# Performance work log

Measured on AMD Instinct MI355X. Metric: run time of the kernel, lower is better.

## Reference

```python
import jax, jax.numpy as jnp
import numpy as np

BS, F, C, H, W = 2, 8, 64, 128, 128
HEADS = 4

def build_edges(bs, f):
    rows, cols, ec = [], [], 0
    for b in range(bs):
        s = b * (2 * f + 2)
        v = list(range(s, s + f)); d = list(range(s + f, s + 2 * f))
        t = s + 2 * f; g = t + 1
        for grp in (v, d, v + d, v + d, v + d + [t], [t], [g]):
            rows += grp; cols += [ec] * len(grp); ec += 1
    return np.asarray(rows, np.int32), np.asarray(cols, np.int32), ec

ROW, COL, NUM_EDGES = build_edges(BS, F)

def conv2d_s2(x, w, b):  # Conv2d k3 s2 p1 + ReLU
    y = jax.lax.conv_general_dilated(x, w, (2, 2), [(1, 1), (1, 1)],
        dimension_numbers=('NCHW', 'OIHW', 'NCHW'))
    return jax.nn.relu(y + b[None, :, None, None])

def conv_t2(x, w, b):  # ConvTranspose2d k3 s2 p1 op1 + ReLU; w: (in,out,3,3)
    wt = jnp.flip(w, (2, 3)).transpose(1, 0, 2, 3)
    y = jax.lax.conv_general_dilated(x, wt, (1, 1), [(1, 2), (1, 2)],
        lhs_dilation=(2, 2), dimension_numbers=('NCHW', 'OIHW', 'NCHW'))
    return jax.nn.relu(y + b[None, :, None, None])

def layer_norm(x, eps=1e-5):  # affine params are default ones/zeros
    mu = x.mean(-1, keepdims=True)
    var = ((x - mu) ** 2).mean(-1, keepdims=True)
    return (x - mu) / jnp.sqrt(var + eps)

def group_norm(x, groups=32, eps=1e-5):
    n, c = x.shape
    xg = x.reshape(n, groups, c // groups)
    mu = xg.mean(-1, keepdims=True)
    var = ((xg - mu) ** 2).mean(-1, keepdims=True)
    return ((xg - mu) / jnp.sqrt(var + eps)).reshape(n, c)

def se_layer(x, w1, w2):  # squeeze over node dim 0
    y = jax.nn.sigmoid(jax.nn.relu(x.mean(0) @ w1.T) @ w2.T)
    return x * y

def hypergraph_conv(x, lin_w, att, edge_w, edge_attr, out_ch):
    # PyG HypergraphConv, use_attention=True, attention_mode='node', heads=4,
    # concat=False, bias=False, eval mode (dropout inactive)
    n = x.shape[0]
    xl = (x @ lin_w.T).reshape(n, HEADS, out_ch)
    ea = (edge_attr @ lin_w.T).reshape(-1, HEADS, out_ch)
    a = (jnp.concatenate([xl[ROW], ea[COL]], axis=-1) * att).sum(-1)  # (E, heads)
    a = jax.nn.leaky_relu(a, 0.2)
    a = jnp.exp(a - jax.ops.segment_max(a, COL, num_segments=NUM_EDGES)[COL])
    a = a / (jax.ops.segment_sum(a, COL, num_segments=NUM_EDGES)[COL] + 1e-16)
    D = jax.ops.segment_sum(edge_w[COL], ROW, num_segments=n)
    D = jnp.where(D > 0, 1.0 / D, 0.0)
    B = jax.ops.segment_sum(jnp.ones(ROW.shape[0], x.dtype), COL, num_segments=NUM_EDGES)
    B = jnp.where(B > 0, 1.0 / B, 0.0)
    e = jax.ops.segment_sum(B[COL][:, None, None] * a[:, :, None] * xl[ROW], COL, num_segments=NUM_EDGES)
    o = jax.ops.segment_sum(D[ROW][:, None, None] * a[:, :, None] * e[COL], ROW, num_segments=n)
    return o.mean(1)  # concat=False -> head mean

def setup_inputs() -> dict:
    key = jax.random.key(0)
    ks = jax.random.split(key, 32)
    def n(k, shape, s=1.0):
        return jax.random.normal(k, shape, jnp.float32) * s
    def u(k, shape):
        return jax.random.uniform(k, shape, jnp.float32)
    return {
        'vision_feat': n(ks[0], (BS, F, C, H, W)), 'vision_pos': n(ks[1], (BS, F, C, H, W), 0.1),
        'motion_feat': n(ks[2], (BS, F, C, H, W)), 'motion_pos': n(ks[3], (BS, F, C, H, W), 0.1),
        'text_feat': n(ks[4], (BS, C, 16)), 'text_pos': n(ks[5], (BS, C, 16), 0.1),
        'cv1_w': n(ks[6], (2 * C, C, 3, 3), 0.04), 'cv1_b': n(ks[7], (2 * C,), 0.01),
        'cv2_w': n(ks[8], (4 * C, 2 * C, 3, 3), 0.03), 'cv2_b': n(ks[9], (4 * C,), 0.01),
        'dc1_w': n(ks[10], (2 * C, C, 3, 3), 0.04), 'dc1_b': n(ks[11], (2 * C,), 0.01),
        'dc2_w': n(ks[12], (4 * C, 2 * C, 3, 3), 0.03), 'dc2_b': n(ks[13], (4 * C,), 0.01),
        'tc1_w': n(ks[14], (4 * C, 2 * C, 3, 3), 0.03), 'tc1_b': n(ks[15], (2 * C,), 0.01),
        'tc2_w': n(ks[16], (2 * C, C, 3, 3), 0.04), 'tc2_b': n(ks[17], (C,), 0.01),
        'lin1_w': n(ks[18], (HEADS * 8 * C, 4 * C), 0.06), 'att1': n(ks[19], (1, HEADS, 16 * C), 0.05),
        'lin2_w': n(ks[20], (HEADS * 4 * C, 8 * C), 0.04), 'att2': n(ks[21], (1, HEADS, 8 * C), 0.05),
        'ew1': u(ks[22], (2 * F * BS + 2,)), 'ew2': u(ks[23], (2 * F * BS + 2,)),
        'ea1': u(ks[24], (2 * F * BS + 2, 4 * C)), 'ea2': u(ks[25], (2 * F * BS + 2, 8 * C)),
        'se1_w1': n(ks[26], (8 * C // 16, 8 * C), 0.06), 'se1_w2': n(ks[27], (8 * C, 8 * C // 16), 0.15),
        'se2_w1': n(ks[28], (4 * C // 16, 4 * C), 0.08), 'se2_w2': n(ks[29], (4 * C, 4 * C // 16), 0.2),
    }

def reference(vision_feat, vision_pos, motion_feat, motion_pos, text_feat, text_pos,
              cv1_w, cv1_b, cv2_w, cv2_b, dc1_w, dc1_b, dc2_w, dc2_b,
              tc1_w, tc1_b, tc2_w, tc2_b, lin1_w, att1, lin2_w, att2,
              ew1, ew2, ea1, ea2, se1_w1, se1_w2, se2_w1, se2_w2):
    bs, f, c, h, w = vision_feat.shape
    # text_pool: AdaptiveMaxPool1d(4) on L=16 -> exact windows of 4; view(bs,-1)
    tn = (text_feat + text_pos).reshape(bs, c, 4, 4).max(-1).reshape(bs, 4 * c)
    v0 = (vision_feat + vision_pos).reshape(bs * f, c, h, w)
    v1 = conv2d_s2(v0, cv1_w, cv1_b)          # (bs*f, 2c, h/2, w/2)
    v2 = conv2d_s2(v1, cv2_w, cv2_b)          # (bs*f, 4c, h/4, w/4)
    vn = layer_norm(v2.max((2, 3)))           # AdaptiveMaxPool2d(1) + LayerNorm
    d0 = (motion_feat + motion_pos).reshape(bs * f, c, h, w)
    dn = layer_norm(conv2d_s2(conv2d_s2(d0, dc1_w, dc1_b), dc2_w, dc2_b).max((2, 3)))
    vb = vn.reshape(bs, f, 4 * c); db = dn.reshape(bs, f, 4 * c)
    obs = tn + (vb + db).mean(1)              # observer = mean(text+v+d) over frames
    x = jnp.concatenate([vb, db, tn[:, None], obs[:, None]], axis=1).reshape(bs * (2 * f + 2), 4 * c)
    x = se_layer(group_norm(jax.nn.relu(hypergraph_conv(x, lin1_w, att1, ew1, ea1, 8 * c))), se1_w1, se1_w2)
    x = se_layer(group_norm(jax.nn.relu(hypergraph_conv(x, lin2_w, att2, ew2, ea2, 4 * c))), se2_w1, se2_w2)
    xb = x.reshape(bs, 2 * f + 2, 4 * c)
    # obs_pool: AdaptiveMaxPool1d(c) on L=4c -> windows of 4
    observers = (tn + xb[:, -1]).reshape(bs, c, 4).max(-1)
    vg = xb[:, :f].reshape(bs * f, 4 * c)
    # bilinear upsample of 1x1 == broadcast; transconv doubles size so the
    # subsequent F.interpolate calls to (h/2,w/2) and (h,w) are identities
    vr = v2 + vg[:, :, None, None]
    vr = v1 + conv_t2(vr, tc1_w, tc1_b)
    vr = v0 + conv_t2(vr, tc2_w, tc2_b)
    return vr, observers
```

## Files before the change

kernel.cpp:

```cpp
#include <hip/hip_runtime.h>
#include <hip/hip_bf16.h>
#include <cstddef>
#include <cstdint>

#define DEV_INLINE __device__ __forceinline__
#define AS1 __attribute__((address_space(1)))
#define AS3 __attribute__((address_space(3)))

typedef __attribute__((ext_vector_type(8))) short short8;
typedef __attribute__((ext_vector_type(4))) float f32x4;
typedef __attribute__((ext_vector_type(2))) float f32x2;
typedef __attribute__((ext_vector_type(4))) unsigned short us4;

DEV_INLINE unsigned short f2bf(float f) {
  uint32_t u = __builtin_bit_cast(uint32_t, f);
  uint32_t r = (u + 0x7fffu + ((u >> 16) & 1u)) >> 16;
  return (unsigned short)r;
}
DEV_INLINE float bf2f(unsigned short u) {
  return __builtin_bit_cast(float, (uint32_t)u << 16);
}

DEV_INLINE void gl_lds16(const float* g, float* l) {
  __builtin_amdgcn_global_load_lds((AS1 void*)const_cast<float*>(g),
                                   (AS3 void*)l, 16, 0, 0);
}

__device__ __constant__ int c_cs[15] = {0,8,16,32,48,65,66,67,75,83,99,115,132,133,134};
__device__ __constant__ int c_row[134] = {
  0,1,2,3,4,5,6,7,
  8,9,10,11,12,13,14,15,
  0,1,2,3,4,5,6,7,8,9,10,11,12,13,14,15,
  0,1,2,3,4,5,6,7,8,9,10,11,12,13,14,15,
  0,1,2,3,4,5,6,7,8,9,10,11,12,13,14,15,16,
  16,
  17,
  18,19,20,21,22,23,24,25,
  26,27,28,29,30,31,32,33,
  18,19,20,21,22,23,24,25,26,27,28,29,30,31,32,33,
  18,19,20,21,22,23,24,25,26,27,28,29,30,31,32,33,
  18,19,20,21,22,23,24,25,26,27,28,29,30,31,32,33,34,
  34,
  35
};
__device__ __constant__ int c_col[134] = {
  0,0,0,0,0,0,0,0,
  1,1,1,1,1,1,1,1,
  2,2,2,2,2,2,2,2,2,2,2,2,2,2,2,2,
  3,3,3,3,3,3,3,3,3,3,3,3,3,3,3,3,
  4,4,4,4,4,4,4,4,4,4,4,4,4,4,4,4,4,
  5,
  6,
  7,7,7,7,7,7,7,7,
  8,8,8,8,8,8,8,8,
  9,9,9,9,9,9,9,9,9,9,9,9,9,9,9,9,
  10,10,10,10,10,10,10,10,10,10,10,10,10,10,10,10,
  11,11,11,11,11,11,11,11,11,11,11,11,11,11,11,11,11,
  12,
  13
};

__global__ __launch_bounds__(512) void k_prep(const float* __restrict__ a,
                                              const float* __restrict__ b,
                                              unsigned short* __restrict__ o) {
  __shared__ float sbuf[32 * 260];
  int bid = blockIdx.x;
  int y = bid & 127, n = bid >> 7;
  int t = threadIdx.x;
  int w = t >> 6, lane = t & 63;
  int cio = lane >> 5;
  int xg4 = (lane & 31) * 4;
  const size_t base = ((size_t)n * 64) * 16384 + (size_t)y * 128;
#pragma unroll
  for (int k = 0; k < 4; ++k) {
    int c = w * 4 + k;
    gl_lds16(a + base + (size_t)(2 * c + cio) * 16384 + xg4, &sbuf[c * 260]);
  }
  __syncthreads();
  auto rd = [&](int ci, int x) {
    return sbuf[(ci >> 1) * 260 + (ci & 1) * 128 + x];
  };
  float av[2][8];
#pragma unroll
  for (int it = 0; it < 2; ++it) {
    int i = t + it * 512;
    int x = i >> 3, cq = i & 7;
#pragma unroll
    for (int j = 0; j < 8; ++j) av[it][j] = rd(cq * 8 + j, x);
  }
  __syncthreads();
#pragma unroll
  for (int k = 0; k < 4; ++k) {
    int c = w * 4 + k;
    gl_lds16(b + base + (size_t)(2 * c + cio) * 16384 + xg4, &sbuf[c * 260]);
  }
  __syncthreads();
  unsigned int* op = (unsigned int*)(o + (((size_t)n * 128 + y) * 128) * 64);
#pragma unroll
  for (int it = 0; it < 2; ++it) {
    int i = t + it * 512;
    int x = i >> 3, cq = i & 7;
    uint4 v;
    unsigned int vv[4];
#pragma unroll
    for (int jj = 0; jj < 4; ++jj) {
      unsigned int lo = f2bf(av[it][2 * jj]     + rd(cq * 8 + 2 * jj, x));
      unsigned int hi = f2bf(av[it][2 * jj + 1] + rd(cq * 8 + 2 * jj + 1, x));
      vv[jj] = lo | (hi << 16);
    }
    v.x = vv[0]; v.y = vv[1]; v.z = vv[2]; v.w = vv[3];
    *reinterpret_cast<uint4*>(op + x * 32 + cq * 4) = v;
  }
}

__global__ void k_wtrans_all(const float* __restrict__ cv1w, const float* __restrict__ dc1w,
                             const float* __restrict__ cv2w, const float* __restrict__ dc2w,
                             const float* __restrict__ tc1w, const float* __restrict__ tc2w,
                             unsigned short* __restrict__ wtb) {
  int idx = blockIdx.x * 256 + threadIdx.x;
  const float* src; int off, lci, lco; bool tra;
  if (idx < 73728)        { src = cv1w; off = 0;       lci = 6; lco = 7; tra = false; }
  else if (idx < 147456)  { src = dc1w; off = 73728;   lci = 6; lco = 7; tra = false; }
  else if (idx < 442368)  { src = cv2w; off = 147456;  lci = 7; lco = 8; tra = false; }
  else if (idx < 737280)  { src = dc2w; off = 442368;  lci = 7; lco = 8; tra = false; }
  else if (idx < 1032192) { src = tc1w; off = 737280;  lci = 8; lco = 7; tra = true;  }
  else if (idx < 1105920) { src = tc2w; off = 1032192; lci = 7; lco = 6; tra = true;  }
  else return;
  int l = idx - off;
  int ci = l & ((1 << lci) - 1);
  int r = l >> lci;
  int co = r & ((1 << lco) - 1);
  int tap = r >> lco;
  size_t si = tra ? (((size_t)ci << lco) + co) * 9 + tap
                  : (((size_t)co << lci) + ci) * 9 + tap;
  wtb[idx] = f2bf(src[si]);
}

template<int CI, int CO, int HO, int WO, int ROUT, bool SPLIT_IN>
__global__ __launch_bounds__(512, 3) void k_conv_mfma_b(
    const unsigned short* __restrict__ in0, const unsigned short* __restrict__ in1,
    const unsigned short* __restrict__ wT0, const unsigned short* __restrict__ wT1,
    const float* __restrict__ b0, const float* __restrict__ b1,
    unsigned short* __restrict__ outn) {
  constexpr int HIN = HO * 2, WIN = WO * 2;
  constexpr int XHP = WO + 2;
  constexpr int R = 2 * ROUT + 1;
  constexpr int NPOS = R * 2 * XHP;
  constexpr int NCH = NPOS * 4;
  constexpr int NCS = CI / 32;
  constexpr int KIT = (NCH + 511) / 512;
  constexpr int CB = CO / 128;
  constexpr int OB = HO / ROUT;
  __shared__ short8 sIn[NPOS * 5];
  int bid = blockIdx.x;
  int cb = bid % CB; bid /= CB;
  int oyb = bid % OB; int n = bid / OB;
  int br = n >> 4;
  const unsigned short* in = SPLIT_IN ? (br ? in1 : in0) : in0;
  const unsigned short* wT = br ? wT1 : wT0;
  const float* bias = br ? b1 : b0;
  int ni = SPLIT_IN ? (n & 15) : n;
  int tid = threadIdx.x;
  int wid = tid >> 6, lane = tid & 63;
  int wm = wid >> 1, wn = wid & 1;
  int llo = lane & 15, lhi = lane >> 4;
  f32x4 acc[2][2] = {};
  const int iy0 = oyb * (2 * ROUT) - 1;
  short8 rv[KIT];
  auto loadr = [&](int cs) {
#pragma unroll
    for (int k = 0; k < KIT; ++k) {
      int i = tid + k * 512;
      short8 v = {};
      if (i < NCH) {
        int c = i & 3, q = i >> 2;
        int xh = q % XHP; int q2 = q / XHP;
        int p = q2 & 1, l = q2 >> 1;
        int x = 2 * xh + p - 1;
        int iy = iy0 + l;
        if (x >= 0 && x < WIN && iy >= 0 && iy < HIN)
          v = *reinterpret_cast<const short8*>(in + ((((size_t)ni * HIN + iy) * WIN + x) * CI + cs * 32 + c * 8));
      }
      rv[k] = v;
    }
  };
  auto writes = [&]() {
#pragma unroll
    for (int k = 0; k < KIT; ++k) {
      int i = tid + k * 512;
      if (i < NCH) sIn[(i >> 2) * 5 + (i & 3)] = rv[k];
    }
  };
  loadr(0);
  for (int cs = 0; cs < NCS; ++cs) {
    writes();
    __syncthreads();
    if (cs + 1 < NCS) loadr(cs + 1);
    short8 afr9[9][2];
#pragma unroll
    for (int tap = 0; tap < 9; ++tap)
#pragma unroll
      for (int m = 0; m < 2; ++m) {
        int co = cb * 128 + wm * 32 + m * 16 + llo;
        afr9[tap][m] = *reinterpret_cast<const short8*>(wT + (((size_t)tap * CO + co) * CI + cs * 32 + lhi * 8));
      }
#pragma unroll
    for (int tap = 0; tap < 9; ++tap) {
      const int ky = tap / 3, kx = tap % 3;
      short8 bfr[2];
#pragma unroll
      for (int n2 = 0; n2 < 2; ++n2) {
        int pix = wn * 32 + n2 * 16 + llo;
        int oyl = (ROUT == 2) ? (pix >> 5) : 0;
        int ox = pix - oyl * WO;
        int lrow = 2 * oyl + ky;
        int pos = (lrow * 2 + (kx & 1)) * XHP + ox + (kx >> 1);
        bfr[n2] = sIn[pos * 5 + lhi];
      }
#pragma unroll
      for (int m = 0; m < 2; ++m)
#pragma unroll
        for (int n2 = 0; n2 < 2; ++n2)
          acc[m][n2] = __builtin_amdgcn_mfma_f32_16x16x32_bf16(afr9[tap][m], bfr[n2], acc[m][n2], 0, 0, 0);
    }
    __syncthreads();
  }
#pragma unroll
  for (int m = 0; m < 2; ++m) {
    int co0 = cb * 128 + wm * 32 + m * 16 + lhi * 4;
    f32x4 bv = *reinterpret_cast<const f32x4*>(bias + co0);
#pragma unroll
    for (int n2 = 0; n2 < 2; ++n2) {
      int pix = wn * 32 + n2 * 16 + llo;
      int oyl = (ROUT == 2) ? (pix >> 5) : 0;
      int ox = pix - oyl * WO;
      int oy = oyb * ROUT + oyl;
      us4 pk;
      pk[0] = f2bf(fmaxf(acc[m][n2][0] + bv[0], 0.f));
      pk[1] = f2bf(fmaxf(acc[m][n2][1] + bv[1], 0.f));
      pk[2] = f2bf(fmaxf(acc[m][n2][2] + bv[2], 0.f));
      pk[3] = f2bf(fmaxf(acc[m][n2][3] + bv[3], 0.f));
      *reinterpret_cast<us4*>(outn + ((((size_t)n * HO + oy) * WO + ox) * CO + co0)) = pk;
    }
  }
}

template<int CI, int CO, int Hi, int Wi, int QR, bool OBF, bool GADD>
__global__ __launch_bounds__(256, 3) void k_deconv_mfma(
    const unsigned short* __restrict__ in,
    const unsigned short* __restrict__ wT,
    const float* __restrict__ bias,
    const unsigned short* __restrict__ resn,
    const float* __restrict__ gsrc,
    unsigned short* __restrict__ outn,
    float* __restrict__ outc) {
  constexpr int QC = 64 / QR;
  constexpr int WP = Wi + 1;
  constexpr int NPOS = (QR + 1) * WP;
  constexpr int NCH = NPOS * 4;
  constexpr int NCS = CI / 32;
  constexpr int KIT = (NCH + 255) / 256;
  constexpr int CB = CO / 64;
  constexpr int OB = Hi / QR;
  constexpr int Ho = Hi * 2, Wo = Wi * 2;
  __shared__ short8 sIn[NPOS * 5];
  int bid = blockIdx.x;
  int cb = bid % CB; bid /= CB;
  int oyb = bid % OB; int n = bid / OB;
  int tid = threadIdx.x;
  int wid = tid >> 6, lane = tid & 63;
  int wm = wid >> 1, wn = wid & 1;
  int llo = lane & 15, lhi = lane >> 4;
  int qy0 = oyb * QR;
  const float* g = nullptr;
  if constexpr (GADD) g = gsrc + ((size_t)((n >> 3) * 18 + (n & 7))) * 256;
  f32x4 acc[4][2][2] = {};
  constexpr int tap_p[9] = {3,2,3,1,0,1,3,2,3};
  constexpr int tap_b[9] = {3,2,2,1,0,0,1,0,0};
  short8 rv[KIT];
  auto loadr = [&](int cs) {
#pragma unroll
    for (int k = 0; k < KIT; ++k) {
      int i = tid + k * 256;
      short8 v = {};
      if (i < NCH) {
        int c = i & 3, q = i >> 2;
        int x = q % WP, l = q / WP;
        int iy = qy0 + l;
        if (x < Wi && iy < Hi) {
          v = *reinterpret_cast<const short8*>(in + (((size_t)(n * Hi + iy) * Wi + x) * CI + cs * 32 + c * 8));
          if constexpr (GADD) {
#pragma unroll
            for (int j = 0; j < 8; ++j) {
              float fv = bf2f((unsigned short)v[j]) + g[cs * 32 + c * 8 + j];
              v[j] = (short)f2bf(fv);
            }
          }
        }
      }
      rv[k] = v;
    }
  };
  auto writes = [&]() {
#pragma unroll
    for (int k = 0; k < KIT; ++k) {
      int i = tid + k * 256;
      if (i < NCH) sIn[(i >> 2) * 5 + (i & 3)] = rv[k];
    }
  };
  loadr(0);
  for (int cs = 0; cs < NCS; ++cs) {
    writes();
    __syncthreads();
    if (cs + 1 < NCS) loadr(cs + 1);
    short8 bfr[2][4];
#pragma unroll
    for (int n2 = 0; n2 < 2; ++n2) {
      int pix = wn * 32 + n2 * 16 + llo;
      int qyl = pix / QC, qx = pix % QC;
#pragma unroll
      for (int bs = 0; bs < 4; ++bs) {
        int pos = (qyl + (bs >> 1)) * WP + qx + (bs & 1);
        bfr[n2][bs] = sIn[pos * 5 + lhi];
      }
    }
#pragma unroll
    for (int m = 0; m < 2; ++m) {
      short8 afr9[9];
#pragma unroll
      for (int tap = 0; tap < 9; ++tap) {
        int co = cb * 64 + wm * 32 + m * 16 + llo;
        afr9[tap] = *reinterpret_cast<const short8*>(wT + (((size_t)tap * CO + co) * CI + cs * 32 + lhi * 8));
      }
#pragma unroll
      for (int tap = 0; tap < 9; ++tap)
#pragma unroll
        for (int n2 = 0; n2 < 2; ++n2)
          acc[tap_p[tap]][m][n2] = __builtin_amdgcn_mfma_f32_16x16x32_bf16(
              afr9[tap], bfr[n2][tap_b[tap]], acc[tap_p[tap]][m][n2], 0, 0, 0);
    }
    __syncthreads();
  }
#pragma unroll
  for (int m = 0; m < 2; ++m) {
    int co0 = cb * 64 + wm * 32 + m * 16 + lhi * 4;
    f32x4 bv = *reinterpret_cast<const f32x4*>(bias + co0);
#pragma unroll
    for (int n2 = 0; n2 < 2; ++n2) {
      int pix = wn * 32 + n2 * 16 + llo;
      int qyl = pix / QC, qx = pix % QC;
      int qy = qy0 + qyl;
      if constexpr (OBF) {
#pragma unroll
        for (int p = 0; p < 4; ++p) {
          int oy = 2 * qy + (p >> 1);
          int ox = 2 * qx + (p & 1);
          size_t ad = ((size_t)(n * Ho + oy) * Wo + ox) * CO + co0;
          us4 r = *reinterpret_cast<const us4*>(resn + ad);
          us4 pk;
#pragma unroll
          for (int c = 0; c < 4; ++c)
            pk[c] = f2bf(bf2f(r[c]) + fmaxf(acc[p][m][n2][c] + bv[c], 0.f));
          *reinterpret_cast<us4*>(outn + ad) = pk;
        }
      } else {
        int qx2 = 2 * qx;
#pragma unroll
        for (int dy = 0; dy < 2; ++dy) {
          int oy = 2 * qy + dy;
          size_t rb = ((size_t)(n * Ho + oy) * Wo + qx2) * CO + co0;
          us4 r0 = *reinterpret_cast<const us4*>(resn + rb);
          us4 r1 = *reinterpret_cast<const us4*>(resn + rb + CO);
#pragma unroll
          for (int c = 0; c < 4; ++c) {
            f32x2 st;
            st[0] = bf2f(r0[c]) + fmaxf(acc[dy * 2][m][n2][c] + bv[c], 0.f);
            st[1] = bf2f(r1[c]) + fmaxf(acc[dy * 2 + 1][m][n2][c] + bv[c], 0.f);
            __builtin_nontemporal_store(st,
                reinterpret_cast<f32x2*>(outc + ((size_t)(n * CO + co0 + c) * Ho + oy) * Wo + qx2));
          }
        }
      }
    }
  }
}

__global__ __launch_bounds__(256) void k_max_part(const unsigned short* __restrict__ x,
                                                  float* __restrict__ pmax) {
  int n = blockIdx.x >> 3, pg = blockIdx.x & 7;
  int t = threadIdx.x;
  int c8 = t & 31;
  int ps = t >> 5;
  const unsigned short* base = x + (size_t)n * 262144 + (size_t)pg * 32768 + (size_t)c8 * 8;
  float m[8];
#pragma unroll
  for (int j = 0; j < 8; ++j) m[j] = -1e30f;
  for (int p = ps * 16; p < ps * 16 + 16; ++p) {
    short8 v = *reinterpret_cast<const short8*>(base + (size_t)p * 256);
#pragma unroll
    for (int j = 0; j < 8; ++j) m[j] = fmaxf(m[j], bf2f((unsigned short)v[j]));
  }
  __shared__ float sred[8][264];
#pragma unroll
  for (int j = 0; j < 8; ++j) sred[ps][c8 * 8 + j] = m[j];
  __syncthreads();
  float mm = sred[0][t];
#pragma unroll
  for (int g = 1; g < 8; ++g) mm = fmaxf(mm, sred[g][t]);
  pmax[((size_t)n * 8 + pg) * 256 + t] = mm;
}

__global__ __launch_bounds__(256) void k_ln(const float* __restrict__ pmax,
                                            float* __restrict__ out) {
  int n = blockIdx.x, ch = threadIdx.x;
  float m = -1e30f;
#pragma unroll
  for (int g = 0; g < 8; ++g)
    m = fmaxf(m, pmax[((size_t)n * 8 + g) * 256 + ch]);
  __shared__ float r1[256], r2[256];
  r1[ch] = m; __syncthreads();
  for (int s = 128; s > 0; s >>= 1) { if (ch < s) r1[ch] += r1[ch + s]; __syncthreads(); }
  float mu = r1[0] * (1.f / 256.f);
  float d = m - mu;
  r2[ch] = d * d; __syncthreads();
  for (int s = 128; s > 0; s >>= 1) { if (ch < s) r2[ch] += r2[ch + s]; __syncthreads(); }
  out[(size_t)n * 256 + ch] = d * rsqrtf(r2[0] * (1.f / 256.f) + 1e-5f);
}

__global__ void k_build_x(const float* __restrict__ tf, const float* __restrict__ tp,
                          const float* __restrict__ nb,
                          float* __restrict__ tn, float* __restrict__ x0) {
  int b = blockIdx.x, ch = threadIdx.x;
  int c4 = ch >> 2, j = ch & 3;
  const float* p = tf + ((size_t)b * 64 + c4) * 16 + j * 4;
  const float* q = tp + ((size_t)b * 64 + c4) * 16 + j * 4;
  float tv = p[0] + q[0];
  tv = fmaxf(tv, p[1] + q[1]);
  tv = fmaxf(tv, p[2] + q[2]);
  tv = fmaxf(tv, p[3] + q[3]);
  tn[(size_t)b * 256 + ch] = tv;
  const float* dn = nb;
  const float* vn = nb + 16 * 256;
  float s = 0.f;
  for (int f = 0; f < 8; ++f) {
    float vv = vn[((size_t)b * 8 + f) * 256 + ch];
    float dd = dn[((size_t)b * 8 + f) * 256 + ch];
    s += vv + dd;
    x0[((size_t)b * 18 + f) * 256 + ch] = vv;
    x0[((size_t)b * 18 + 8 + f) * 256 + ch] = dd;
  }
  x0[((size_t)b * 18 + 16) * 256 + ch] = tv;
  x0[((size_t)b * 18 + 17) * 256 + ch] = tv + s * (1.f / 8.f);
}

__global__ __launch_bounds__(256) void k_gnn_lin(
    const float* __restrict__ x, const float* __restrict__ ea,
    const float* __restrict__ w, float* __restrict__ y, int K, int M) {
  int chunks = M >> 8;
  int r = blockIdx.x / chunks;
  int ob = (blockIdx.x % chunks) * 256 + threadIdx.x;
  const float* src = (r < 36) ? (x + (size_t)r * K) : (ea + (size_t)(r - 36) * K);
  __shared__ __align__(16) float sxr[512];
  for (int k = threadIdx.x; k < K; k += 256) sxr[k] = src[k];
  __syncthreads();
  const float4* w4 = reinterpret_cast<const float4*>(w + (size_t)ob * K);
  const float4* x4 = reinterpret_cast<const float4*>(sxr);
  float acc = 0.f;
  int k4 = K >> 2;
  for (int k = 0; k < k4; ++k) {
    float4 a = x4[k], b = w4[k];
    acc += a.x * b.x + a.y * b.y + a.z * b.z + a.w * b.w;
  }
  y[(size_t)r * M + ob] = acc;
}

template<int OC>
__global__ __launch_bounds__(256) void k_gnn_attsm(
    const float* __restrict__ y, const float* __restrict__ att,
    float* __restrict__ attw) {
  int t = threadIdx.x;
  __shared__ float sx_s[144], seb_s[60];
  __shared__ float a_s[536];
  if (t < 200) {
    int r = t >> 2, h = t & 3;
    const float4* row = reinterpret_cast<const float4*>(y + ((size_t)r * 4 + h) * OC);
    const float4* ar = reinterpret_cast<const float4*>(att + (size_t)h * 2 * OC + (r < 36 ? 0 : OC));
    float s = 0.f;
#pragma unroll 4
    for (int k = 0; k < OC / 4; ++k) {
      float4 a = row[k], b = ar[k];
      s += a.x * b.x + a.y * b.y + a.z * b.z + a.w * b.w;
    }
    if (r < 36) sx_s[r * 4 + h] = s; else seb_s[(r - 36) * 4 + h] = s;
  }
  __syncthreads();
  for (int idx = t; idx < 536; idx += 256) {
    int i = idx >> 2, h = idx & 3;
    float v = sx_s[c_row[i] * 4 + h] + seb_s[c_col[i] * 4 + h];
    a_s[idx] = (v > 0.f) ? v : 0.2f * v;
  }
  __syncthreads();
  if (t < 56) {
    int c = t >> 2, h = t & 3;
    int st = c_cs[c], en = c_cs[c + 1];
    float m = -1e30f;
    for (int i = st; i < en; ++i) m = fmaxf(m, a_s[i * 4 + h]);
    float s = 0.f;
    for (int i = st; i < en; ++i) { float e = __expf(a_s[i * 4 + h] - m); a_s[i * 4 + h] = e; s += e; }
    float inv = 1.f / (s + 1e-16f);
    for (int i = st; i < en; ++i) a_s[i * 4 + h] *= inv;
  }
  __syncthreads();
  for (int idx = t; idx < 536; idx += 256) attw[idx] = a_s[idx];
}

template<int OC>
__global__ __launch_bounds__(256) void k_edge_agg(
    const float* __restrict__ y, const float* __restrict__ attw,
    float* __restrict__ eb) {
  int idx = blockIdx.x * 256 + threadIdx.x;
  if (idx >= 14 * 4 * OC) return;
  int ch = idx % OC;
  int h = (idx / OC) & 3;
  int c = idx / (4 * OC);
  int st = c_cs[c], en = c_cs[c + 1];
  float s = 0.f;
  for (int i = st; i < en; ++i)
    s += attw[i * 4 + h] * y[(size_t)c_row[i] * (4 * OC) + h * OC + ch];
  eb[idx] = s * (1.f / (float)(en - st));
}

template<int OC>
__global__ __launch_bounds__(256) void k_node_agg(
    const float* __restrict__ attw, const float* __restrict__ eb,
    const float* __restrict__ ew, float* __restrict__ ho) {
  int idx = blockIdx.x * 256 + threadIdx.x;
  if (idx >= 36 * OC) return;
  int ch = idx % OC;
  int node = idx / OC;
  int b = node / 18, ln = node % 18;
  int ncols, cols[4], gis[4];
  if (ln < 16) {
    ncols = 4;
    cols[0] = b * 7 + (ln < 8 ? 0 : 1); gis[0] = b * 67 + ln;
    cols[1] = b * 7 + 2; gis[1] = b * 67 + 16 + ln;
    cols[2] = b * 7 + 3; gis[2] = b * 67 + 32 + ln;
    cols[3] = b * 7 + 4; gis[3] = b * 67 + 48 + ln;
  } else if (ln == 16) {
    ncols = 2;
    cols[0] = b * 7 + 4; gis[0] = b * 67 + 64;
    cols[1] = b * 7 + 5; gis[1] = b * 67 + 65;
    cols[2] = cols[3] = 0; gis[2] = gis[3] = 0;
  } else {
    ncols = 1;
    cols[0] = b * 7 + 6; gis[0] = b * 67 + 66;
    cols[1] = cols[2] = cols[3] = 0; gis[1] = gis[2] = gis[3] = 0;
  }
  float dsum = 0.f;
#pragma unroll
  for (int k = 0; k < 4; ++k) if (k < ncols) dsum += ew[cols[k]];
  float D = dsum > 0.f ? 1.f / dsum : 0.f;
  float s = 0.f;
#pragma unroll
  for (int k = 0; k < 4; ++k) {
    if (k < ncols) {
#pragma unroll
      for (int h = 0; h < 4; ++h)
        s += attw[gis[k] * 4 + h] * eb[((size_t)cols[k] * 4 + h) * OC + ch];
    }
  }
  ho[idx] = fmaxf(0.25f * D * s, 0.f);
}

template<int C, int Cr>
__global__ __launch_bounds__(512) void k_gn_se(
    const float* __restrict__ hin, const float* __restrict__ w1,
    const float* __restrict__ w2, float* __restrict__ x) {
  int t = threadIdx.x;
  constexpr int gs = C >> 5;
  for (int idx = t; idx < 36 * 32; idx += 512) {
    int node = idx >> 5, g = idx & 31;
    const float* p = hin + (size_t)node * C + g * gs;
    float s = 0.f, s2 = 0.f;
#pragma unroll
    for (int k = 0; k < gs; ++k) { float v = p[k]; s += v; s2 += v * v; }
    float mu = s * (1.f / gs);
    float var = s2 * (1.f / gs) - mu * mu;
    float inv = rsqrtf(fmaxf(var, 0.f) + 1e-5f);
    float* q = x + (size_t)node * C + g * gs;
#pragma unroll
    for (int k = 0; k < gs; ++k) q[k] = (p[k] - mu) * inv;
  }
  __threadfence_block();
  __syncthreads();
  __shared__ float smean[C];
  __shared__ float spart[Cr][17];
  __shared__ float shid[Cr];
  __shared__ float sscale[C];
  if (t < C) {
    float s = 0.f;
    for (int nn = 0; nn < 36; ++nn) s += x[(size_t)nn * C + t];
    smean[t] = s * (1.f / 36.f);
  }
  __syncthreads();
  if (t < Cr * 16) {
    int hid = t >> 4, sub = t & 15;
    constexpr int CH = C / 16;
    float s = 0.f;
#pragma unroll
    for (int k = 0; k < CH; ++k)
      s += w1[(size_t)hid * C + sub * CH + k] * smean[sub * CH + k];
    spart[hid][sub] = s;
  }
  __syncthreads();
  if (t < Cr) {
    float s = 0.f;
#pragma unroll
    for (int k = 0; k < 16; ++k) s += spart[t][k];
    shid[t] = fmaxf(s, 0.f);
  }
  __syncthreads();
  if (t < C) {
    float s = 0.f;
#pragma unroll
    for (int k = 0; k < Cr; ++k) s += w2[(size_t)t * Cr + k] * shid[k];
    sscale[t] = 1.f / (1.f + __expf(-s));
  }
  __syncthreads();
  for (int idx = t; idx < 36 * C; idx += 512) x[idx] *= sscale[idx % C];
}

__global__ void k_obs(const float* __restrict__ tn, const float* __restrict__ x2,
                      float* __restrict__ out) {
  int t = threadIdx.x;
  if (t >= 128) return;
  int b = t >> 6, ch = t & 63;
  const float* a = tn + (size_t)b * 256 + ch * 4;
  const float* c = x2 + ((size_t)b * 18 + 17) * 256 + ch * 4;
  float m = a[0] + c[0];
  m = fmaxf(m, a[1] + c[1]);
  m = fmaxf(m, a[2] + c[2]);
  m = fmaxf(m, a[3] + c[3]);
  out[b * 64 + ch] = m;
}

extern "C" void kernel_launch(void* const* d_in, const int* in_sizes, int n_in,
                              void* d_out, int out_size, void* d_ws, size_t ws_size,
                              hipStream_t stream) {
  (void)in_sizes; (void)n_in; (void)out_size; (void)ws_size;
  const float* vf    = (const float*)d_in[0];
  const float* vp    = (const float*)d_in[1];
  const float* mf    = (const float*)d_in[2];
  const float* mp    = (const float*)d_in[3];
  const float* tf    = (const float*)d_in[4];
  const float* tp    = (const float*)d_in[5];
  const float* cv1w  = (const float*)d_in[6];
  const float* cv1b  = (const float*)d_in[7];
  const float* cv2w  = (const float*)d_in[8];
  const float* cv2b  = (const float*)d_in[9];
  const float* dc1w  = (const float*)d_in[10];
  const float* dc1b  = (const float*)d_in[11];
  const float* dc2w  = (const float*)d_in[12];
  const float* dc2b  = (const float*)d_in[13];
  const float* tc1w  = (const float*)d_in[14];
  const float* tc1b  = (const float*)d_in[15];
  const float* tc2w  = (const float*)d_in[16];
  const float* tc2b  = (const float*)d_in[17];
  const float* lin1w = (const float*)d_in[18];
  const float* att1  = (const float*)d_in[19];
  const float* lin2w = (const float*)d_in[20];
  const float* att2  = (const float*)d_in[21];
  const float* ew1   = (const float*)d_in[22];
  const float* ew2   = (const float*)d_in[23];
  const float* ea1   = (const float*)d_in[24];
  const float* ea2   = (const float*)d_in[25];
  const float* se1w1 = (const float*)d_in[26];
  const float* se1w2 = (const float*)d_in[27];
  const float* se2w1 = (const float*)d_in[28];
  const float* se2w2 = (const float*)d_in[29];

  float* ws  = (float*)d_ws;
  float* out = (float*)d_out;

  unsigned short* p0nm = (unsigned short*)(ws);
  unsigned short* p0nv = (unsigned short*)(ws + 8388608);
  unsigned short* q1nb = (unsigned short*)(ws + 16777216);
  unsigned short* wtb  = (unsigned short*)(ws + 25165824);
  float* sm   = ws + 25718784;
  float* tn   = sm;
  float* nb   = sm + 512;
  float* x0   = sm + 8704;
  float* xl   = sm + 17920;
  float* eb   = sm + 120520;
  float* ho   = sm + 149192;
  float* x1   = sm + 167624;
  float* x2   = sm + 186056;
  float* attw = sm + 195272;
  float* pmax = sm + 195904;

  unsigned short* v2nb = (unsigned short*)d_out;
  unsigned short* t1n = (unsigned short*)(ws);

  unsigned short* wTc1 = wtb;
  unsigned short* wTd1 = wtb + 73728;
  unsigned short* wTc2 = wtb + 147456;
  unsigned short* wTd2 = wtb + 442368;
  unsigned short* wTt1 = wtb + 737280;
  unsigned short* wTt2 = wtb + 1032192;

  k_wtrans_all<<<4320, 256, 0, stream>>>(cv1w, dc1w, cv2w, dc2w, tc1w, tc2w, wtb);

  k_prep<<<2048, 512, 0, stream>>>(mf, mp, p0nm);
  k_prep<<<2048, 512, 0, stream>>>(vf, vp, p0nv);

  k_conv_mfma_b<64, 128, 64, 64, 1, true><<<2048, 512, 0, stream>>>(
      p0nm, p0nv, wTd1, wTc1, dc1b, cv1b, q1nb);
  k_conv_mfma_b<128, 256, 32, 32, 2, false><<<1024, 512, 0, stream>>>(
      q1nb, nullptr, wTd2, wTc2, dc2b, cv2b, v2nb);
  k_max_part<<<256, 256, 0, stream>>>(v2nb, pmax);
  k_ln<<<32, 256, 0, stream>>>(pmax, nb);

  k_build_x<<<2, 256, 0, stream>>>(tf, tp, nb, tn, x0);

  k_gnn_lin<<<50 * 8, 256, 0, stream>>>(x0, ea1, lin1w, xl, 256, 2048);
  k_gnn_attsm<512><<<1, 256, 0, stream>>>(xl, att1, attw);
  k_edge_agg<512><<<112, 256, 0, stream>>>(xl, attw, eb);
  k_node_agg<512><<<72, 256, 0, stream>>>(attw, eb, ew1, ho);
  k_gn_se<512, 32><<<1, 512, 0, stream>>>(ho, se1w1, se1w2, x1);

  k_gnn_lin<<<50 * 4, 256, 0, stream>>>(x1, ea2, lin2w, xl, 512, 1024);
  k_gnn_attsm<256><<<1, 256, 0, stream>>>(xl, att2, attw);
  k_edge_agg<256><<<56, 256, 0, stream>>>(xl, attw, eb);
  k_node_agg<256><<<36, 256, 0, stream>>>(attw, eb, ew2, ho);
  k_gn_se<256, 16><<<1, 512, 0, stream>>>(ho, se2w1, se2w2, x2);

  k_obs<<<1, 128, 0, stream>>>(tn, x2, out + 16777216);

  unsigned short* v2nv = v2nb + 4194304;
  unsigned short* q1nv = q1nb + 8388608;
  k_deconv_mfma<256, 128, 32, 32, 2, true, true><<<512, 256, 0, stream>>>(
      v2nv, wTt1, tc1b, q1nv, x2, t1n, nullptr);
  k_deconv_mfma<128, 64, 64, 64, 1, false, false><<<1024, 256, 0, stream>>>(
      t1n, wTt2, tc2b, p0nv, nullptr, nullptr, out);
}
```

Before: 462.4 us.

## Drop LDS staging in stride-2 convs and load input fragments directly from global

```diff
diff --git a/kernel.cpp b/kernel.cpp
--- a/kernel.cpp
+++ b/kernel.cpp
@@ -137,21 +137,15 @@
 }
 
 template<int CI, int CO, int HO, int WO, int ROUT, bool SPLIT_IN>
-__global__ __launch_bounds__(512, 3) void k_conv_mfma_b(
+__global__ __launch_bounds__(512, 4) void k_conv_direct(
     const unsigned short* __restrict__ in0, const unsigned short* __restrict__ in1,
     const unsigned short* __restrict__ wT0, const unsigned short* __restrict__ wT1,
     const float* __restrict__ b0, const float* __restrict__ b1,
     unsigned short* __restrict__ outn) {
   constexpr int HIN = HO * 2, WIN = WO * 2;
-  constexpr int XHP = WO + 2;
-  constexpr int R = 2 * ROUT + 1;
-  constexpr int NPOS = R * 2 * XHP;
-  constexpr int NCH = NPOS * 4;
   constexpr int NCS = CI / 32;
-  constexpr int KIT = (NCH + 511) / 512;
   constexpr int CB = CO / 128;
   constexpr int OB = HO / ROUT;
-  __shared__ short8 sIn[NPOS * 5];
   int bid = blockIdx.x;
   int cb = bid % CB; bid /= CB;
   int oyb = bid % OB; int n = bid / OB;
@@ -164,66 +158,43 @@
   int wid = tid >> 6, lane = tid & 63;
   int wm = wid >> 1, wn = wid & 1;
   int llo = lane & 15, lhi = lane >> 4;
+  int ox_[2], iyb_[2];
+#pragma unroll
+  for (int n2 = 0; n2 < 2; ++n2) {
+    int pix = wn * 32 + n2 * 16 + llo;
+    int oyl = (ROUT == 2) ? (pix >> 5) : 0;
+    int ox = pix - oyl * WO;
+    int oy = oyb * ROUT + oyl;
+    ox_[n2] = ox;
+    iyb_[n2] = 2 * oy - 1;
+  }
   f32x4 acc[2][2] = {};
-  const int iy0 = oyb * (2 * ROUT) - 1;
-  short8 rv[KIT];
-  auto loadr = [&](int cs) {
-#pragma unroll
-    for (int k = 0; k < KIT; ++k) {
-      int i = tid + k * 512;
-      short8 v = {};
-      if (i < NCH) {
-        int c = i & 3, q = i >> 2;
-        int xh = q % XHP; int q2 = q / XHP;
-        int p = q2 & 1, l = q2 >> 1;
-        int x = 2 * xh + p - 1;
-        int iy = iy0 + l;
-        if (x >= 0 && x < WIN && iy >= 0 && iy < HIN)
-          v = *reinterpret_cast<const short8*>(in + ((((size_t)ni * HIN + iy) * WIN + x) * CI + cs * 32 + c * 8));
-      }
-      rv[k] = v;
-    }
-  };
-  auto writes = [&]() {
-#pragma unroll
-    for (int k = 0; k < KIT; ++k) {
-      int i = tid + k * 512;
-      if (i < NCH) sIn[(i >> 2) * 5 + (i & 3)] = rv[k];
-    }
-  };
-  loadr(0);
   for (int cs = 0; cs < NCS; ++cs) {
-    writes();
-    __syncthreads();
-    if (cs + 1 < NCS) loadr(cs + 1);
-    short8 afr9[9][2];
-#pragma unroll
-    for (int tap = 0; tap < 9; ++tap)
+    int kb = cs * 32 + lhi * 8;
+#pragma unroll
+    for (int tap = 0; tap < 9; ++tap) {
+      const int ky = tap / 3, kx = tap % 3;
+      short8 afr[2], bfr[2];
 #pragma unroll
       for (int m = 0; m < 2; ++m) {
         int co = cb * 128 + wm * 32 + m * 16 + llo;
-        afr9[tap][m] = *reinterpret_cast<const short8*>(wT + (((size_t)tap * CO + co) * CI + cs * 32 + lhi * 8));
+        afr[m] = *reinterpret_cast<const short8*>(wT + (((size_t)tap * CO + co) * CI + kb));
       }
 #pragma unroll
-    for (int tap = 0; tap < 9; ++tap) {
-      const int ky = tap / 3, kx = tap % 3;
-      short8 bfr[2];
-#pragma unroll
       for (int n2 = 0; n2 < 2; ++n2) {
-        int pix = wn * 32 + n2 * 16 + llo;
-        int oyl = (ROUT == 2) ? (pix >> 5) : 0;
-        int ox = pix - oyl * WO;
-        int lrow = 2 * oyl + ky;
-        int pos = (lrow * 2 + (kx & 1)) * XHP + ox + (kx >> 1);
-        bfr[n2] = sIn[pos * 5 + lhi];
+        int ix = 2 * ox_[n2] - 1 + kx;
+        int iy = iyb_[n2] + ky;
+        short8 v = {};
+        if (ix >= 0 && iy >= 0)
+          v = *reinterpret_cast<const short8*>(in + ((((size_t)ni * HIN + iy) * WIN + ix) * CI + kb));
+        bfr[n2] = v;
       }
 #pragma unroll
       for (int m = 0; m < 2; ++m)
 #pragma unroll
         for (int n2 = 0; n2 < 2; ++n2)
-          acc[m][n2] = __builtin_amdgcn_mfma_f32_16x16x32_bf16(afr9[tap][m], bfr[n2], acc[m][n2], 0, 0, 0);
-    }
-    __syncthreads();
+          acc[m][n2] = __builtin_amdgcn_mfma_f32_16x16x32_bf16(afr[m], bfr[n2], acc[m][n2], 0, 0, 0);
+    }
   }
 #pragma unroll
   for (int m = 0; m < 2; ++m) {
@@ -713,9 +684,9 @@
   k_prep<<<2048, 512, 0, stream>>>(mf, mp, p0nm);
   k_prep<<<2048, 512, 0, stream>>>(vf, vp, p0nv);
 
-  k_conv_mfma_b<64, 128, 64, 64, 1, true><<<2048, 512, 0, stream>>>(
+  k_conv_direct<64, 128, 64, 64, 1, true><<<2048, 512, 0, stream>>>(
       p0nm, p0nv, wTd1, wTc1, dc1b, cv1b, q1nb);
-  k_conv_mfma_b<128, 256, 32, 32, 2, false><<<1024, 512, 0, stream>>>(
+  k_conv_direct<128, 256, 32, 32, 2, false><<<1024, 512, 0, stream>>>(
       q1nb, nullptr, wTd2, wTc2, dc2b, cv2b, v2nb);
   k_max_part<<<256, 256, 0, stream>>>(v2nb, pmax);
   k_ln<<<32, 256, 0, stream>>>(pmax, nb);
```

After: 565.5 us. 22.3% more time.
